# Performance work log

Hardware: AMD Instinct MI355X
Metric: run time of the kernel (lower is better)

## Reference

```python
import jax, jax.numpy as jnp
import numpy as np

NUM_BINS = 64
R = 2                      # kernel_radius = ceil(2*sigma), sigma=1
NB = NUM_BINS + 2 * R      # 68 padded bins
EPS = 1e-8


def _bspline(d):
    # cubic B-spline Parzen kernel, sigma=1 so d/sigma == d
    ad = jnp.abs(d)
    return jnp.where(
        ad < 1.0, (3.0 * ad ** 3 - 6.0 * ad ** 2 + 4.0) / 6.0,
        jnp.where(ad < 2.0, (2.0 - ad) ** 3 / 6.0, jnp.zeros_like(ad)))


def setup_inputs() -> dict:
    key = jax.random.key(0)
    k1, k2 = jax.random.split(key)
    shape = (2, 1, 80, 80, 80)
    source = jax.random.normal(k1, shape, dtype=jnp.float32)
    target = jax.random.normal(k2, shape, dtype=jnp.float32)
    return {"source": source, "target": target}


def _win(x):
    # x: [B, N] flattened voxels (mask=None, sample_rate=1 keeps all voxels)
    # returns win_idx [B, 2R, N] int32 and bspline weights [B, 2R, N]
    mx = jax.lax.stop_gradient(jnp.max(x, axis=1))            # [B]
    mn = jax.lax.stop_gradient(jnp.min(x, axis=1))            # [B]
    bw = (mx - mn) / NUM_BINS                                 # bin width
    pad_min = mn - bw * R
    pos = (x - pad_min[:, None]) / bw[:, None]                # [B, N]
    idx = jax.lax.stop_gradient(
        jnp.clip(jnp.floor(pos), R, R + NUM_BINS - 1))        # detached floor+clamp
    min_win = (idx - R + 1).astype(jnp.int32)                 # [B, N]
    r = jnp.arange(2 * R, dtype=jnp.int32)                    # [2R]
    win_idx = min_win[:, None, :] + r[None, :, None]          # [B, 2R, N]
    # bin_center is arange(NB), so gathered centers == win_idx as float
    w = _bspline(pos[:, None, :] - win_idx.astype(x.dtype))   # [B, 2R, N]
    return win_idx, w


def _densify(win_idx, w):
    # scatter-add window weights into dense [B, NB, N] bin-weight matrix.
    # (Equivalent to the torch eq-mask-and-sum loop: window indices are distinct.)
    B, _, N = w.shape
    col = jnp.broadcast_to(jnp.arange(N), win_idx.shape[1:])  # [2R, N]
    def per_b(ib, wb):
        return jnp.zeros((NB, N), wb.dtype).at[ib, col].add(wb)
    return jax.vmap(per_b)(win_idx, w)


def reference(source, target):
    B = source.shape[0]
    s = source.reshape(B, -1)   # [B, N]
    t = target.reshape(B, -1)
    si, sw = _win(s)
    ti, tw = _win(t)
    sbw = _densify(si, sw)      # [B, NB, N]
    tbw = _densify(ti, tw)      # [B, NB, N]
    source_hist = sbw.sum(-1)   # [B, NB]
    target_hist = tbw.sum(-1)
    joint_hist = jnp.einsum('bin,bjn->bij', sbw, tbw)   # [B, NB, NB]
    source_density = source_hist / jnp.maximum(source_hist.sum(-1, keepdims=True), EPS)
    target_density = target_hist / jnp.maximum(target_hist.sum(-1, keepdims=True), EPS)
    joint_density = joint_hist / jnp.maximum(joint_hist.sum(axis=(1, 2), keepdims=True), EPS)
    return (source_density, target_density, joint_density)
```

## Files before the change

### kernel.cpp

```cpp
#include <hip/hip_runtime.h>
#include <float.h>

#define NB 68
#define NJ (NB * NB)
#define NSLICE 4
#define HTPB 1024
#define MMBLK 125
#define SCALE 16384.0f
#define LHSZ (2 * NJ + 8)


__global__ __launch_bounds__(1024) void k_prep(const float* __restrict__ src,
                                               const float* __restrict__ tgt,
                                               float4* __restrict__ P,
                                               unsigned* __restrict__ J,
                                               unsigned* __restrict__ ctr,
                                               int n4) {
    __shared__ float red[16][4];
    const int b = blockIdx.y;
    const int lin = (b * gridDim.x + blockIdx.x) * 1024 + threadIdx.x;
    if (lin < NSLICE * 2 * NJ) J[lin] = 0u;
    else if (lin == NSLICE * 2 * NJ) { ctr[0] = 0u; ctr[1] = 0u; }

    const int i = blockIdx.x * 1024 + threadIdx.x;
    float smx = -FLT_MAX, smn = FLT_MAX, tmx = -FLT_MAX, tmn = FLT_MAX;
    if (i < n4) {
        float4 v = ((const float4*)src)[(size_t)b * n4 + i];
        float4 w = ((const float4*)tgt)[(size_t)b * n4 + i];
        smx = fmaxf(fmaxf(v.x, v.y), fmaxf(v.z, v.w));
        smn = fminf(fminf(v.x, v.y), fminf(v.z, v.w));
        tmx = fmaxf(fmaxf(w.x, w.y), fmaxf(w.z, w.w));
        tmn = fminf(fminf(w.x, w.y), fminf(w.z, w.w));
    }
#pragma unroll
    for (int m = 1; m < 64; m <<= 1) {
        smx = fmaxf(smx, __shfl_xor(smx, m));
        smn = fminf(smn, __shfl_xor(smn, m));
        tmx = fmaxf(tmx, __shfl_xor(tmx, m));
        tmn = fminf(tmn, __shfl_xor(tmn, m));
    }
    const int wave = threadIdx.x >> 6;
    if ((threadIdx.x & 63) == 0) {
        red[wave][0] = smx;
        red[wave][1] = smn;
        red[wave][2] = tmx;
        red[wave][3] = tmn;
    }
    __syncthreads();
    if (threadIdx.x == 0) {
#pragma unroll
        for (int k = 1; k < 16; ++k) {
            smx = fmaxf(smx, red[k][0]);
            smn = fminf(smn, red[k][1]);
            tmx = fmaxf(tmx, red[k][2]);
            tmn = fminf(tmn, red[k][3]);
        }
        P[b * 128 + blockIdx.x] = make_float4(smx, smn, tmx, tmn);
    }
}

__device__ __forceinline__ float bspl(float d) {
    float ad = fabsf(d);
    float a = (3.0f * ad * ad * ad - 6.0f * ad * ad + 4.0f) * (1.0f / 6.0f);
    float t = 2.0f - ad;
    float c = t * t * t * (1.0f / 6.0f);
    return ad < 1.0f ? a : (ad < 2.0f ? c : 0.0f);
}

__device__ __forceinline__ void vox1(float sv, float tv, unsigned* lh,
                                     float spad, float sinv, float tpad,
                                     float tinv) {
    float posS = (sv - spad) * sinv;
    float fS = floorf(posS);
    fS = fminf(fmaxf(fS, 2.0f), 65.0f);
    int si = (int)fS - 1;
    float dS = posS - fS;
    float a[4] = {bspl(dS + 1.0f), bspl(dS), bspl(dS - 1.0f), bspl(dS - 2.0f)};

    float posT = (tv - tpad) * tinv;
    float fT = floorf(posT);
    fT = fminf(fmaxf(fT, 2.0f), 65.0f);
    int ti = (int)fT - 1;
    float dT = posT - fT;
    float b0 = bspl(dT + 1.0f), b1 = bspl(dT), b2 = bspl(dT - 1.0f),
          b3 = bspl(dT - 2.0f);

    unsigned* base = lh + ((ti & 1) ? (NJ + 1) : 0) + si * NB + ti;
#pragma unroll
    for (int r = 0; r < 4; ++r) {
        unsigned q0 = (unsigned)(a[r] * b0 * SCALE + 0.5f);
        unsigned q1 = (unsigned)(a[r] * b1 * SCALE + 0.5f);
        unsigned q2 = (unsigned)(a[r] * b2 * SCALE + 0.5f);
        unsigned q3 = (unsigned)(a[r] * b3 * SCALE + 0.5f);
        atomicAdd((unsigned long long*)(base + r * NB),
                  (unsigned long long)q0 | ((unsigned long long)q1 << 32));
        atomicAdd((unsigned long long*)(base + r * NB + 2),
                  (unsigned long long)q2 | ((unsigned long long)q3 << 32));
    }
}

__global__ __launch_bounds__(HTPB) void k_hist(
    const float* __restrict__ src, const float* __restrict__ tgt,
    const float4* __restrict__ P, unsigned* __restrict__ J,
    unsigned* __restrict__ ctr, float* __restrict__ out, double inv, int n4) {
    __shared__ __align__(16) unsigned lh[LHSZ];
    __shared__ float pmm[8], mmv[4];
    __shared__ unsigned lastFlag;
    const int tid = threadIdx.x;
    const int b = blockIdx.y;

    if (tid < 128) {
        float smx = -FLT_MAX, smn = FLT_MAX, tmx = -FLT_MAX, tmn = FLT_MAX;
        if (tid < MMBLK) {
            float4 v = P[b * 128 + tid];
            smx = v.x; smn = v.y; tmx = v.z; tmn = v.w;
        }
#pragma unroll
        for (int m = 1; m < 64; m <<= 1) {
            smx = fmaxf(smx, __shfl_xor(smx, m));
            smn = fminf(smn, __shfl_xor(smn, m));
            tmx = fmaxf(tmx, __shfl_xor(tmx, m));
            tmn = fminf(tmn, __shfl_xor(tmn, m));
        }
        if ((tid & 63) == 0) {
            int w = tid >> 6;
            pmm[w * 4 + 0] = smx;
            pmm[w * 4 + 1] = smn;
            pmm[w * 4 + 2] = tmx;
            pmm[w * 4 + 3] = tmn;
        }
    }
    uint4* z4 = (uint4*)lh;
    const uint4 zz = make_uint4(0u, 0u, 0u, 0u);
    for (int i = tid; i < LHSZ / 4; i += HTPB) z4[i] = zz;
    __syncthreads();
    if (tid == 0) {
        mmv[0] = fmaxf(pmm[0], pmm[4]);
        mmv[1] = fminf(pmm[1], pmm[5]);
        mmv[2] = fmaxf(pmm[2], pmm[6]);
        mmv[3] = fminf(pmm[3], pmm[7]);
    }
    __syncthreads();

    const float sbw = (mmv[0] - mmv[1]) * (1.0f / 64.0f);
    const float tbw = (mmv[2] - mmv[3]) * (1.0f / 64.0f);
    const float sinv = 1.0f / sbw, tinv = 1.0f / tbw;
    const float spad = mmv[1] - 2.0f * sbw;
    const float tpad = mmv[3] - 2.0f * tbw;

    const int i0 = blockIdx.x * HTPB + tid;
    if (i0 < n4) {
        float4 sA = ((const float4*)src)[(size_t)b * n4 + i0];
        float4 tA = ((const float4*)tgt)[(size_t)b * n4 + i0];
        vox1(sA.x, tA.x, lh, spad, sinv, tpad, tinv);
        vox1(sA.y, tA.y, lh, spad, sinv, tpad, tinv);
        vox1(sA.z, tA.z, lh, spad, sinv, tpad, tinv);
        vox1(sA.w, tA.w, lh, spad, sinv, tpad, tinv);
    }
    __syncthreads();

    const int rot = (blockIdx.x * 1327) % NJ;
    unsigned* Jb = J + ((size_t)(blockIdx.x & (NSLICE - 1)) * 2 + b) * NJ;
    for (int k = tid; k < NJ; k += HTPB) {
        int i = k + rot;
        if (i >= NJ) i -= NJ;
        unsigned s = lh[i] + lh[NJ + 1 + i];
        if (s) atomicAdd(&Jb[i], s);
    }
    __syncthreads();

    if (tid == 0)
        lastFlag = (atomicAdd(&ctr[b], 1u) == (unsigned)(MMBLK - 1)) ? 1u : 0u;
    __syncthreads();
    if (!lastFlag) return;

    float* jf = (float*)lh;
    float* part = (float*)(lh + NJ + 16);
    for (int i = tid; i < NJ; i += HTPB) {
        unsigned s = 0u;
#pragma unroll
        for (int sl = 0; sl < NSLICE; ++sl)
            s += __hip_atomic_load(&J[((size_t)sl * 2 + b) * NJ + i],
                                   __ATOMIC_RELAXED, __HIP_MEMORY_SCOPE_AGENT);
        float f = (float)((double)s * inv);
        jf[i] = f;
        out[4 * NB + b * NJ + i] = f;
    }
    __syncthreads();

    if (tid < 8 * NB) {
        int r = tid >> 3, k = tid & 7;
        float s = 0.0f;
#pragma unroll
        for (int j = 0; j < 9; ++j) {
            int c = k + 8 * j;
            if (c < NB) s += jf[r * NB + c];
        }
        part[r * 8 + k] = s;
    }
    __syncthreads();
    if (tid < NB) {
        float s = part[tid * 8 + 0] + part[tid * 8 + 1] + part[tid * 8 + 2] +
                  part[tid * 8 + 3] + part[tid * 8 + 4] + part[tid * 8 + 5] +
                  part[tid * 8 + 6] + part[tid * 8 + 7];
        out[b * NB + tid] = s;
    }
    __syncthreads();

    if (tid < 8 * NB) {
        int c = tid >> 3, k = tid & 7;
        float s = 0.0f;
#pragma unroll
        for (int j = 0; j < 9; ++j) {
            int r = k + 8 * j;
            if (r < NB) s += jf[r * NB + c];
        }
        part[c * 8 + k] = s;
    }
    __syncthreads();
    if (tid < NB) {
        float s = part[tid * 8 + 0] + part[tid * 8 + 1] + part[tid * 8 + 2] +
                  part[tid * 8 + 3] + part[tid * 8 + 4] + part[tid * 8 + 5] +
                  part[tid * 8 + 6] + part[tid * 8 + 7];
        out[2 * NB + b * NB + tid] = s;
    }
}

extern "C" void kernel_launch(void* const* d_in, const int* in_sizes, int n_in,
                              void* d_out, int out_size, void* d_ws,
                              size_t ws_size, hipStream_t stream) {
    const float* src = (const float*)d_in[0];
    const float* tgt = (const float*)d_in[1];
    float* out = (float*)d_out;
    unsigned* ctr = (unsigned*)d_ws;
    float4* P = (float4*)((char*)d_ws + 64);
    unsigned* J = (unsigned*)((char*)d_ws + 4160);
    const int nvox = in_sizes[0] / 2;
    const int n4 = nvox / 4;
    const double inv = 1.0 / ((double)nvox * (double)SCALE);

    k_prep<<<dim3(MMBLK, 2), dim3(1024), 0, stream>>>(src, tgt, P, J, ctr, n4);
    k_hist<<<dim3(MMBLK, 2), dim3(HTPB), 0, stream>>>(src, tgt, P, J, ctr, out,
                                                      inv, n4);
}
```

Measured before the change: 22.85 us.

## Fuse min/max prep and histogram kernels using a grid-wide spin barrier

Merges the separate min/max reduction kernel into the histogram kernel. Each block publishes its partial min/max, increments a per-batch counter and spins until all blocks have arrived, then reduces the partials and builds the histogram from registers it already loaded. This removes one kernel launch and the second read of the inputs. In exchange it adds a memset, relies on all 250 blocks being co-resident for the spin barrier, and moves the J zeroing into the same kernel that later accumulates into J.

```diff
diff --git a/kernel.cpp b/kernel.cpp
--- a/kernel.cpp
+++ b/kernel.cpp
@@ -4,60 +4,12 @@
 #define NB 68
 #define NJ (NB * NB)
 #define NSLICE 4
-#define HTPB 1024
-#define MMBLK 125
+#define TPB 1024
+#define BXB 125
 #define SCALE 16384.0f
 #define LHSZ (2 * NJ + 8)
-
-
-__global__ __launch_bounds__(1024) void k_prep(const float* __restrict__ src,
-                                               const float* __restrict__ tgt,
-                                               float4* __restrict__ P,
-                                               unsigned* __restrict__ J,
-                                               unsigned* __restrict__ ctr,
-                                               int n4) {
-    __shared__ float red[16][4];
-    const int b = blockIdx.y;
-    const int lin = (b * gridDim.x + blockIdx.x) * 1024 + threadIdx.x;
-    if (lin < NSLICE * 2 * NJ) J[lin] = 0u;
-    else if (lin == NSLICE * 2 * NJ) { ctr[0] = 0u; ctr[1] = 0u; }
-
-    const int i = blockIdx.x * 1024 + threadIdx.x;
-    float smx = -FLT_MAX, smn = FLT_MAX, tmx = -FLT_MAX, tmn = FLT_MAX;
-    if (i < n4) {
-        float4 v = ((const float4*)src)[(size_t)b * n4 + i];
-        float4 w = ((const float4*)tgt)[(size_t)b * n4 + i];
-        smx = fmaxf(fmaxf(v.x, v.y), fmaxf(v.z, v.w));
-        smn = fminf(fminf(v.x, v.y), fminf(v.z, v.w));
-        tmx = fmaxf(fmaxf(w.x, w.y), fmaxf(w.z, w.w));
-        tmn = fminf(fminf(w.x, w.y), fminf(w.z, w.w));
-    }
-#pragma unroll
-    for (int m = 1; m < 64; m <<= 1) {
-        smx = fmaxf(smx, __shfl_xor(smx, m));
-        smn = fminf(smn, __shfl_xor(smn, m));
-        tmx = fmaxf(tmx, __shfl_xor(tmx, m));
-        tmn = fminf(tmn, __shfl_xor(tmn, m));
-    }
-    const int wave = threadIdx.x >> 6;
-    if ((threadIdx.x & 63) == 0) {
-        red[wave][0] = smx;
-        red[wave][1] = smn;
-        red[wave][2] = tmx;
-        red[wave][3] = tmn;
-    }
-    __syncthreads();
-    if (threadIdx.x == 0) {
-#pragma unroll
-        for (int k = 1; k < 16; ++k) {
-            smx = fmaxf(smx, red[k][0]);
-            smn = fminf(smn, red[k][1]);
-            tmx = fmaxf(tmx, red[k][2]);
-            tmn = fminf(tmn, red[k][3]);
-        }
-        P[b * 128 + blockIdx.x] = make_float4(smx, smn, tmx, tmn);
-    }
-}
+#define ZWORDS ((NSLICE * NJ + BXB - 1) / BXB)
+
 
 __device__ __forceinline__ float bspl(float d) {
     float ad = fabsf(d);
@@ -99,40 +51,112 @@
     }
 }
 
-__global__ __launch_bounds__(HTPB) void k_hist(
+__global__ __launch_bounds__(TPB) void k_all(
     const float* __restrict__ src, const float* __restrict__ tgt,
-    const float4* __restrict__ P, unsigned* __restrict__ J,
+    unsigned* __restrict__ P, unsigned* __restrict__ J,
     unsigned* __restrict__ ctr, float* __restrict__ out, double inv, int n4) {
     __shared__ __align__(16) unsigned lh[LHSZ];
+    __shared__ float red[16][4];
     __shared__ float pmm[8], mmv[4];
     __shared__ unsigned lastFlag;
-    const int tid = threadIdx.x;
-    const int b = blockIdx.y;
+    const int tid = threadIdx.x, bx = blockIdx.x, b = blockIdx.y;
+
+    const int i0 = bx * TPB + tid;
+    const bool valid = i0 < n4;
+    float4 sv = make_float4(0.f, 0.f, 0.f, 0.f);
+    float4 tv = make_float4(0.f, 0.f, 0.f, 0.f);
+    if (valid) {
+        sv = ((const float4*)src)[(size_t)b * n4 + i0];
+        tv = ((const float4*)tgt)[(size_t)b * n4 + i0];
+    }
+    uint4* z4 = (uint4*)lh;
+    const uint4 zz = make_uint4(0u, 0u, 0u, 0u);
+    for (int i = tid; i < LHSZ / 4; i += TPB) z4[i] = zz;
+    if (tid < ZWORDS) {
+        int g = bx * ZWORDS + tid;
+        if (g < NSLICE * NJ) {
+            int sl = g / NJ, i = g - sl * NJ;
+            __hip_atomic_store(&J[((size_t)sl * 2 + b) * NJ + i], 0u,
+                               __ATOMIC_RELAXED, __HIP_MEMORY_SCOPE_AGENT);
+        }
+    }
+
+    float smx = -FLT_MAX, smn = FLT_MAX, tmx = -FLT_MAX, tmn = FLT_MAX;
+    if (valid) {
+        smx = fmaxf(fmaxf(sv.x, sv.y), fmaxf(sv.z, sv.w));
+        smn = fminf(fminf(sv.x, sv.y), fminf(sv.z, sv.w));
+        tmx = fmaxf(fmaxf(tv.x, tv.y), fmaxf(tv.z, tv.w));
+        tmn = fminf(fminf(tv.x, tv.y), fminf(tv.z, tv.w));
+    }
+#pragma unroll
+    for (int m = 1; m < 64; m <<= 1) {
+        smx = fmaxf(smx, __shfl_xor(smx, m));
+        smn = fminf(smn, __shfl_xor(smn, m));
+        tmx = fmaxf(tmx, __shfl_xor(tmx, m));
+        tmn = fminf(tmn, __shfl_xor(tmn, m));
+    }
+    const int wave = tid >> 6;
+    if ((tid & 63) == 0) {
+        red[wave][0] = smx;
+        red[wave][1] = smn;
+        red[wave][2] = tmx;
+        red[wave][3] = tmn;
+    }
+    __syncthreads();
+
+    if (tid == 0) {
+#pragma unroll
+        for (int k = 1; k < 16; ++k) {
+            smx = fmaxf(smx, red[k][0]);
+            smn = fminf(smn, red[k][1]);
+            tmx = fmaxf(tmx, red[k][2]);
+            tmn = fminf(tmn, red[k][3]);
+        }
+        const unsigned pb = (unsigned)(b * 128 + bx) * 4u;
+        __hip_atomic_store(&P[pb + 0], __float_as_uint(smx), __ATOMIC_RELAXED,
+                           __HIP_MEMORY_SCOPE_AGENT);
+        __hip_atomic_store(&P[pb + 1], __float_as_uint(smn), __ATOMIC_RELAXED,
+                           __HIP_MEMORY_SCOPE_AGENT);
+        __hip_atomic_store(&P[pb + 2], __float_as_uint(tmx), __ATOMIC_RELAXED,
+                           __HIP_MEMORY_SCOPE_AGENT);
+        __hip_atomic_store(&P[pb + 3], __float_as_uint(tmn), __ATOMIC_RELAXED,
+                           __HIP_MEMORY_SCOPE_AGENT);
+        __hip_atomic_fetch_add(&ctr[b], 1u, __ATOMIC_RELEASE,
+                               __HIP_MEMORY_SCOPE_AGENT);
+        while (__hip_atomic_load(&ctr[b], __ATOMIC_RELAXED,
+                                 __HIP_MEMORY_SCOPE_AGENT) < (unsigned)BXB) {
+        }
+    }
+    __syncthreads();
 
     if (tid < 128) {
-        float smx = -FLT_MAX, smn = FLT_MAX, tmx = -FLT_MAX, tmn = FLT_MAX;
-        if (tid < MMBLK) {
-            float4 v = P[b * 128 + tid];
-            smx = v.x; smn = v.y; tmx = v.z; tmn = v.w;
+        float a = -FLT_MAX, c = FLT_MAX, d = -FLT_MAX, e = FLT_MAX;
+        if (tid < BXB) {
+            const unsigned pb = (unsigned)(b * 128 + tid) * 4u;
+            a = __uint_as_float(__hip_atomic_load(&P[pb + 0], __ATOMIC_RELAXED,
+                                                  __HIP_MEMORY_SCOPE_AGENT));
+            c = __uint_as_float(__hip_atomic_load(&P[pb + 1], __ATOMIC_RELAXED,
+                                                  __HIP_MEMORY_SCOPE_AGENT));
+            d = __uint_as_float(__hip_atomic_load(&P[pb + 2], __ATOMIC_RELAXED,
+                                                  __HIP_MEMORY_SCOPE_AGENT));
+            e = __uint_as_float(__hip_atomic_load(&P[pb + 3], __ATOMIC_RELAXED,
+                                                  __HIP_MEMORY_SCOPE_AGENT));
         }
 #pragma unroll
         for (int m = 1; m < 64; m <<= 1) {
-            smx = fmaxf(smx, __shfl_xor(smx, m));
-            smn = fminf(smn, __shfl_xor(smn, m));
-            tmx = fmaxf(tmx, __shfl_xor(tmx, m));
-            tmn = fminf(tmn, __shfl_xor(tmn, m));
+            a = fmaxf(a, __shfl_xor(a, m));
+            c = fminf(c, __shfl_xor(c, m));
+            d = fmaxf(d, __shfl_xor(d, m));
+            e = fminf(e, __shfl_xor(e, m));
         }
         if ((tid & 63) == 0) {
             int w = tid >> 6;
-            pmm[w * 4 + 0] = smx;
-            pmm[w * 4 + 1] = smn;
-            pmm[w * 4 + 2] = tmx;
-            pmm[w * 4 + 3] = tmn;
-        }
-    }
-    uint4* z4 = (uint4*)lh;
-    const uint4 zz = make_uint4(0u, 0u, 0u, 0u);
-    for (int i = tid; i < LHSZ / 4; i += HTPB) z4[i] = zz;
+            pmm[w * 4 + 0] = a;
+            pmm[w * 4 + 1] = c;
+            pmm[w * 4 + 2] = d;
+            pmm[w * 4 + 3] = e;
+        }
+    }
     __syncthreads();
     if (tid == 0) {
         mmv[0] = fmaxf(pmm[0], pmm[4]);
@@ -148,20 +172,17 @@
     const float spad = mmv[1] - 2.0f * sbw;
     const float tpad = mmv[3] - 2.0f * tbw;
 
-    const int i0 = blockIdx.x * HTPB + tid;
-    if (i0 < n4) {
-        float4 sA = ((const float4*)src)[(size_t)b * n4 + i0];
-        float4 tA = ((const float4*)tgt)[(size_t)b * n4 + i0];
-        vox1(sA.x, tA.x, lh, spad, sinv, tpad, tinv);
-        vox1(sA.y, tA.y, lh, spad, sinv, tpad, tinv);
-        vox1(sA.z, tA.z, lh, spad, sinv, tpad, tinv);
-        vox1(sA.w, tA.w, lh, spad, sinv, tpad, tinv);
-    }
-    __syncthreads();
-
-    const int rot = (blockIdx.x * 1327) % NJ;
-    unsigned* Jb = J + ((size_t)(blockIdx.x & (NSLICE - 1)) * 2 + b) * NJ;
-    for (int k = tid; k < NJ; k += HTPB) {
+    if (valid) {
+        vox1(sv.x, tv.x, lh, spad, sinv, tpad, tinv);
+        vox1(sv.y, tv.y, lh, spad, sinv, tpad, tinv);
+        vox1(sv.z, tv.z, lh, spad, sinv, tpad, tinv);
+        vox1(sv.w, tv.w, lh, spad, sinv, tpad, tinv);
+    }
+    __syncthreads();
+
+    const int rot = (bx * 1327) % NJ;
+    unsigned* Jb = J + ((size_t)(bx & (NSLICE - 1)) * 2 + b) * NJ;
+    for (int k = tid; k < NJ; k += TPB) {
         int i = k + rot;
         if (i >= NJ) i -= NJ;
         unsigned s = lh[i] + lh[NJ + 1 + i];
@@ -170,13 +191,17 @@
     __syncthreads();
 
     if (tid == 0)
-        lastFlag = (atomicAdd(&ctr[b], 1u) == (unsigned)(MMBLK - 1)) ? 1u : 0u;
+        lastFlag = (__hip_atomic_fetch_add(&ctr[2 + b], 1u, __ATOMIC_RELEASE,
+                                           __HIP_MEMORY_SCOPE_AGENT) ==
+                    (unsigned)(BXB - 1))
+                       ? 1u
+                       : 0u;
     __syncthreads();
     if (!lastFlag) return;
 
     float* jf = (float*)lh;
     float* part = (float*)(lh + NJ + 16);
-    for (int i = tid; i < NJ; i += HTPB) {
+    for (int i = tid; i < NJ; i += TPB) {
         unsigned s = 0u;
 #pragma unroll
         for (int sl = 0; sl < NSLICE; ++sl)
@@ -233,13 +258,13 @@
     const float* tgt = (const float*)d_in[1];
     float* out = (float*)d_out;
     unsigned* ctr = (unsigned*)d_ws;
-    float4* P = (float4*)((char*)d_ws + 64);
+    unsigned* P = (unsigned*)((char*)d_ws + 64);
     unsigned* J = (unsigned*)((char*)d_ws + 4160);
     const int nvox = in_sizes[0] / 2;
     const int n4 = nvox / 4;
     const double inv = 1.0 / ((double)nvox * (double)SCALE);
 
-    k_prep<<<dim3(MMBLK, 2), dim3(1024), 0, stream>>>(src, tgt, P, J, ctr, n4);
-    k_hist<<<dim3(MMBLK, 2), dim3(HTPB), 0, stream>>>(src, tgt, P, J, ctr, out,
-                                                      inv, n4);
-}
+    hipMemsetAsync(ctr, 0, 16, stream);
+    k_all<<<dim3(BXB, 2), dim3(TPB), 0, stream>>>(src, tgt, P, J, ctr, out,
+                                                  inv, n4);
+}
```

Result: slower. 31.18 us (+36.5%).
